# Optimization experiments

Measured on AMD Instinct MI355X. Metric: run time of the kernel, lower is better.

## Reference

```python
import jax, jax.numpy as jnp
import numpy as np

DIM = 768
D_STATE = 64
D_CONV = 4
EXPAND = 2
D_INNER = EXPAND * DIM          # 1536
DT_RANK = (DIM + 15) // 16      # 48
BATCH = 2
SEQ = 1024
EPS = 1e-5


def setup_inputs() -> dict:
    key = jax.random.key(0)
    ks = jax.random.split(key, 10)
    s = 0.02
    x = jax.random.normal(ks[0], (BATCH, SEQ, DIM), dtype=jnp.float32)
    gamma = jnp.ones((DIM,), jnp.float32)
    beta = jnp.zeros((DIM,), jnp.float32)
    W_in = jax.random.normal(ks[1], (2 * D_INNER, DIM), jnp.float32) * s
    conv_w = jax.random.normal(ks[2], (D_INNER, D_CONV), jnp.float32) * s
    conv_b = jnp.zeros((D_INNER,), jnp.float32)
    W_x = jax.random.normal(ks[3], (DT_RANK + 2 * D_STATE, D_INNER), jnp.float32) * s
    W_dt = jax.random.normal(ks[4], (D_INNER, DT_RANK), jnp.float32) * s
    b_dt = jax.random.uniform(ks[5], (D_INNER,), jnp.float32, -4.0, -2.0)  # dt bias ~ log-space init
    # S4D-real init: A_log[d, n] = log(n+1)
    A_log = jnp.log(jnp.broadcast_to(jnp.arange(1, D_STATE + 1, dtype=jnp.float32), (D_INNER, D_STATE)))
    D = jnp.ones((D_INNER,), jnp.float32)
    W_out = jax.random.normal(ks[6], (DIM, D_INNER), jnp.float32) * s
    return {"x": x, "gamma": gamma, "beta": beta, "W_in": W_in,
            "conv_w": conv_w, "conv_b": conv_b, "W_x": W_x,
            "W_dt": W_dt, "b_dt": b_dt, "A_log": A_log, "D": D, "W_out": W_out}


def _silu(v):
    return v * jax.nn.sigmoid(v)


def _mamba_forward(x, gamma, beta, W_in, conv_w, conv_b, W_x, W_dt, b_dt, A_log, D, W_out):
    B, L, _ = x.shape
    # LayerNorm
    mu = jnp.mean(x, axis=-1, keepdims=True)
    var = jnp.mean(jnp.square(x - mu), axis=-1, keepdims=True)
    xn = (x - mu) * jax.lax.rsqrt(var + EPS) * gamma + beta
    # in_proj -> (u, z)
    xz = jnp.einsum('bld,ed->ble', xn, W_in)          # [B, L, 2*D_INNER]
    u, z = jnp.split(xz, 2, axis=-1)                  # each [B, L, D_INNER]
    # depthwise causal conv1d along L
    uc = jnp.transpose(u, (0, 2, 1))                  # [B, C, L]
    uc = jnp.pad(uc, ((0, 0), (0, 0), (D_CONV - 1, 0)))
    kern = conv_w[:, None, :]                         # [C, 1, K]
    uc = jax.lax.conv_general_dilated(
        uc, kern, window_strides=(1,), padding='VALID',
        feature_group_count=D_INNER,
        dimension_numbers=('NCH', 'OIH', 'NCH'))
    uc = uc + conv_b[None, :, None]
    u = _silu(jnp.transpose(uc, (0, 2, 1)))           # [B, L, D_INNER]
    # x_proj -> (dt, Bssm, Cssm)
    x_dbl = jnp.einsum('blc,ec->ble', u, W_x)
    dt = x_dbl[..., :DT_RANK]
    Bssm = x_dbl[..., DT_RANK:DT_RANK + D_STATE]      # [B, L, N]
    Cssm = x_dbl[..., DT_RANK + D_STATE:]             # [B, L, N]
    delta = jax.nn.softplus(jnp.einsum('blr,cr->blc', dt, W_dt) + b_dt)  # [B, L, C]
    A = -jnp.exp(A_log)                               # [C, N]

    # selective scan, time-major
    d_t = jnp.transpose(delta, (1, 0, 2))             # [L, B, C]
    B_t = jnp.transpose(Bssm, (1, 0, 2))              # [L, B, N]
    C_t = jnp.transpose(Cssm, (1, 0, 2))              # [L, B, N]
    u_t = jnp.transpose(u, (1, 0, 2))                 # [L, B, C]

    def step(h, inp):
        d, b, c, uu = inp
        dA = jnp.exp(d[..., None] * A)                # [B, C, N]
        h = dA * h + d[..., None] * b[:, None, :] * uu[..., None]
        y = jnp.sum(h * c[:, None, :], axis=-1) + D * uu
        return h, y

    h0 = jnp.zeros((B, D_INNER, D_STATE), x.dtype)
    _, ys = jax.lax.scan(step, h0, (d_t, B_t, C_t, u_t))
    y = jnp.transpose(ys, (1, 0, 2))                  # [B, L, C]
    y = y * _silu(z)
    return jnp.einsum('blc,dc->bld', y, W_out)


def reference(x, gamma, beta, W_in, conv_w, conv_b, W_x, W_dt, b_dt, A_log, D, W_out):
    return _mamba_forward(x, gamma, beta, W_in, conv_w, conv_b, W_x,
                          W_dt, b_dt, A_log, D, W_out)
```

## Files before the change

kernel.cpp:

```cpp
#include <hip/hip_runtime.h>
#include <math.h>

#define DIMD 768
#define DSTATE 64
#define DINNER 1536
#define DTRANK 48
#define BATCH 2
#define SEQL 1024
#define NTOK (BATCH*SEQL)
#define XDBL_P 192
#define EPSV 1e-5f

typedef __attribute__((ext_vector_type(8))) short bf16x8;
typedef __attribute__((ext_vector_type(4))) float f32x4;

__device__ inline short f2bf(float f) {
  unsigned u = __float_as_uint(f);
  u = u + 0x7FFFu + ((u >> 16) & 1u);
  return (short)(u >> 16);
}

__global__ __launch_bounds__(256) void ln_kernel(const float* __restrict__ x,
                                                 const float* __restrict__ gamma,
                                                 const float* __restrict__ beta,
                                                 short* __restrict__ xnq) {
  int wave = threadIdx.x >> 6;
  int lane = threadIdx.x & 63;
  int row = blockIdx.x * 4 + wave;
  if (row >= NTOK) return;
  const float* xr = x + (size_t)row * DIMD;
  float v[12];
  float s = 0.f, ss = 0.f;
#pragma unroll
  for (int i = 0; i < 12; ++i) {
    v[i] = xr[lane + i*64];
    s += v[i];
    ss += v[i]*v[i];
  }
#pragma unroll
  for (int m = 1; m < 64; m <<= 1) {
    s  += __shfl_xor(s, m);
    ss += __shfl_xor(ss, m);
  }
  float mu   = s * (1.f/DIMD);
  float var  = ss * (1.f/DIMD) - mu*mu;
  float rstd = rsqrtf(var + EPSV);
  short* o = xnq + (size_t)row * DIMD;
#pragma unroll
  for (int i = 0; i < 12; ++i) {
    int j = lane + i*64;
    o[j] = f2bf((v[i] - mu) * rstd * gamma[j] + beta[j]);
  }
}

#define NW_IN  (3072*768)
#define NW_OUT (768*1536)
#define NW_XP  (192*1536)
__global__ __launch_bounds__(256) void cvt_weights_kernel(const float* __restrict__ Win,
                                                          const float* __restrict__ Wout,
                                                          const float* __restrict__ Wx,
                                                          short* __restrict__ qin,
                                                          short* __restrict__ qout,
                                                          short* __restrict__ qx) {
  int idx = blockIdx.x * 256 + threadIdx.x;
  if (idx < NW_IN) { qin[idx] = f2bf(Win[idx]); return; }
  idx -= NW_IN;
  if (idx < NW_OUT) { qout[idx] = f2bf(Wout[idx]); return; }
  idx -= NW_OUT;
  if (idx < NW_XP) {
    int r = idx / 1536;
    qx[idx] = (r < 176) ? f2bf(Wx[idx]) : (short)0;
  }
}

template<int BN>
__global__ __launch_bounds__(256) void gemm_mfma(const short* __restrict__ A,
                                                 const short* __restrict__ B,
                                                 float* __restrict__ C, int ldc,
                                                 int Kfull, int Kchunk, size_t partStride) {
  constexpr int BM = 128, BK = 64;
  constexpr int WN = (BN == 128) ? 2 : 1;
  constexpr int WM = 4 / WN;
  constexpr int MFR = BM / (WM * 16);
  constexpr int NFR = BN / (WN * 16);
  constexpr int BSW = (BN * BK * 2) / 4096;
  __shared__ short As[BM * BK];
  __shared__ short Bs[BN * BK];
  const int tid  = threadIdx.x;
  const int wave = tid >> 6, lane = tid & 63;
  const int m0 = blockIdx.y * BM;
  const int n0 = blockIdx.x * BN;
  const int wm = wave / WN, wn = wave % WN;
  const int kBeg = blockIdx.z * Kchunk;
  const int kEnd = kBeg + Kchunk;
  C += (size_t)blockIdx.z * partStride;

  const short* aSrc = A + (size_t)(m0 + (tid >> 3)) * Kfull + (tid & 7) * 8;
  const short* bSrc = B + (size_t)(n0 + (tid >> 3)) * Kfull + (tid & 7) * 8;

  f32x4 acc[MFR][NFR];
#pragma unroll
  for (int i = 0; i < MFR; ++i)
#pragma unroll
    for (int j = 0; j < NFR; ++j)
      acc[i][j] = (f32x4){0.f, 0.f, 0.f, 0.f};

  for (int k0 = kBeg; k0 < kEnd; k0 += BK) {
#pragma unroll
    for (int s = 0; s < 4; ++s)
      __builtin_amdgcn_global_load_lds(
        (const __attribute__((address_space(1))) void*)(aSrc + (size_t)s*32*Kfull + k0),
        (__attribute__((address_space(3))) void*)((char*)As + s*4096 + wave*1024),
        16, 0, 0);
#pragma unroll
    for (int s = 0; s < BSW; ++s)
      __builtin_amdgcn_global_load_lds(
        (const __attribute__((address_space(1))) void*)(bSrc + (size_t)s*32*Kfull + k0),
        (__attribute__((address_space(3))) void*)((char*)Bs + s*4096 + wave*1024),
        16, 0, 0);
    __syncthreads();

#pragma unroll
    for (int kk = 0; kk < 2; ++kk) {
      bf16x8 af[MFR], bfr[NFR];
#pragma unroll
      for (int i = 0; i < MFR; ++i) {
        int r = wm * (BM / WM) + i * 16 + (lane & 15);
        af[i] = *(const bf16x8*)&As[r * BK + kk * 32 + (lane >> 4) * 8];
      }
#pragma unroll
      for (int j = 0; j < NFR; ++j) {
        int r = wn * (BN / WN) + j * 16 + (lane & 15);
        bfr[j] = *(const bf16x8*)&Bs[r * BK + kk * 32 + (lane >> 4) * 8];
      }
#pragma unroll
      for (int i = 0; i < MFR; ++i)
#pragma unroll
        for (int j = 0; j < NFR; ++j)
          acc[i][j] = __builtin_amdgcn_mfma_f32_16x16x32_bf16(af[i], bfr[j], acc[i][j], 0, 0, 0);
    }
    __syncthreads();
  }

  const int cn = lane & 15, cr4 = (lane >> 4) * 4;
#pragma unroll
  for (int i = 0; i < MFR; ++i)
#pragma unroll
    for (int j = 0; j < NFR; ++j)
#pragma unroll
      for (int r = 0; r < 4; ++r) {
        int m = m0 + wm * (BM / WM) + i * 16 + cr4 + r;
        int n = n0 + wn * (BN / WN) + j * 16 + cn;
        C[(size_t)m * ldc + n] = acc[i][j][r];
      }
}

__global__ __launch_bounds__(256) void reduce4_kernel(const float* __restrict__ p,
                                                      float* __restrict__ outb) {
  const int n4 = NTOK * XDBL_P / 4;
  int i = blockIdx.x * 256 + threadIdx.x;
  if (i >= n4) return;
  const float4* p4 = (const float4*)p;
  float4 a = p4[i];
  float4 b = p4[i + n4];
  float4 c = p4[i + 2*n4];
  float4 d = p4[i + 3*n4];
  float4 r;
  r.x = ((a.x + b.x) + c.x) + d.x;
  r.y = ((a.y + b.y) + c.y) + d.y;
  r.z = ((a.z + b.z) + c.z) + d.z;
  r.w = ((a.w + b.w) + c.w) + d.w;
  ((float4*)outb)[i] = r;
}

template<int ACT>
__global__ __launch_bounds__(256) void gemm_nt(const float* __restrict__ A, int lda,
                                               const float* __restrict__ W, int ldw,
                                               const float* __restrict__ bias,
                                               float* __restrict__ C, int ldc,
                                               int M, int N, int K) {
  __shared__ float Asl[16][68];
  __shared__ float Wsl[16][68];
  int tid = threadIdx.x;
  int m0 = blockIdx.y * 64;
  int n0 = blockIdx.x * 64;
  int lrow = tid >> 2;
  int lq   = tid & 3;
  int tx = tid & 15;
  int ty = tid >> 4;
  float acc[4][4] = {{0.f}};

  for (int k0 = 0; k0 < K; k0 += 16) {
    float4 av = make_float4(0.f,0.f,0.f,0.f);
    int ar = m0 + lrow;
    if (ar < M) av = *(const float4*)(A + (size_t)ar*lda + k0 + lq*4);
    float4 wv = make_float4(0.f,0.f,0.f,0.f);
    int wr = n0 + lrow;
    if (wr < N) wv = *(const float4*)(W + (size_t)wr*ldw + k0 + lq*4);
    __syncthreads();
    Asl[lq*4+0][lrow] = av.x; Asl[lq*4+1][lrow] = av.y;
    Asl[lq*4+2][lrow] = av.z; Asl[lq*4+3][lrow] = av.w;
    Wsl[lq*4+0][lrow] = wv.x; Wsl[lq*4+1][lrow] = wv.y;
    Wsl[lq*4+2][lrow] = wv.z; Wsl[lq*4+3][lrow] = wv.w;
    __syncthreads();
#pragma unroll
    for (int kk = 0; kk < 16; ++kk) {
      float4 a4 = *(const float4*)&Asl[kk][ty*4];
      float4 w4 = *(const float4*)&Wsl[kk][tx*4];
      float a[4] = {a4.x, a4.y, a4.z, a4.w};
      float w[4] = {w4.x, w4.y, w4.z, w4.w};
#pragma unroll
      for (int i = 0; i < 4; ++i)
#pragma unroll
        for (int j = 0; j < 4; ++j)
          acc[i][j] += a[i]*w[j];
    }
  }

#pragma unroll
  for (int i = 0; i < 4; ++i) {
    int m = m0 + ty*4 + i;
    if (m >= M) continue;
    float* crow = C + (size_t)m*ldc;
    float bm = (ACT == 2) ? bias[m] : 0.f;
#pragma unroll
    for (int j = 0; j < 4; ++j) {
      int n = n0 + tx*4 + j;
      if (n >= N) continue;
      float val = acc[i][j];
      if (ACT == 2) {
        val += bm;
        val = (val > 20.f) ? val : log1pf(__expf(val));
      }
      crow[n] = val;
    }
  }
}

__global__ __launch_bounds__(256) void conv_silu_kernel(const float* __restrict__ xz,
                                                        const float* __restrict__ conv_w,
                                                        const float* __restrict__ conv_b,
                                                        float* __restrict__ uT,
                                                        short* __restrict__ ucq) {
  __shared__ float tile[64][65];
  int b  = blockIdx.z;
  int c0 = blockIdx.x * 64;
  int t0 = blockIdx.y * 64;
  int lx = threadIdx.x & 63;
  int ly = threadIdx.x >> 6;
  int c = c0 + lx;
  const int S = 2*DINNER;
  float w0 = conv_w[c*4+0], w1 = conv_w[c*4+1], w2 = conv_w[c*4+2], w3 = conv_w[c*4+3];
  float cb = conv_b[c];
#pragma unroll
  for (int i = 0; i < 16; ++i) {
    int tl = ly*16 + i;
    int t = t0 + tl;
    const float* up = xz + ((size_t)b*SEQL + t) * S + c;
    float acc = cb + up[0]*w3;
    if (t >= 1) acc += up[-1*S]*w2;
    if (t >= 2) acc += up[-2*S]*w1;
    if (t >= 3) acc += up[-3*S]*w0;
    float sig = 1.f / (1.f + __expf(-acc));
    float v = acc * sig;
    ucq[((size_t)b*SEQL + t)*DINNER + c] = f2bf(v);
    tile[lx][tl] = v;
  }
  __syncthreads();
#pragma unroll
  for (int i = 0; i < 16; ++i) {
    int cl = ly*16 + i;
    uT[((size_t)(c0 + cl))*NTOK + (size_t)b*SEQL + t0 + lx] = tile[cl][lx];
  }
}

__device__ inline float readlane_f(float v, int l) {
  return __int_as_float(__builtin_amdgcn_readlane(__float_as_int(v), l));
}

__global__ __launch_bounds__(256) void scan_kernel(const float* __restrict__ dT,
                                                   const float* __restrict__ x_dbl,
                                                   const float* __restrict__ uT,
                                                   const float* __restrict__ A_log,
                                                   const float* __restrict__ Dp,
                                                   float* __restrict__ yT) {
  __shared__ float red_all[4][32*66 + 32];
  int tid  = threadIdx.x;
  int wave = tid >> 6;
  int lane = tid & 63;
  float* red = red_all[wave];
  int ch = blockIdx.x * 4 + wave;
  int b = ch / DINNER;
  int c = ch % DINNER;
  float Ac = -__expf(A_log[(size_t)c*64 + lane]);
  float Dc = Dp[c];
  float h = 0.f;
  const float* dp = dT + (size_t)c * NTOK + (size_t)b * SEQL;
  const float* up = uT + (size_t)c * NTOK + (size_t)b * SEQL;
  float* yrow = yT + ((size_t)b*DINNER + c) * SEQL;
  const float* xB = x_dbl + ((size_t)b * SEQL) * XDBL_P + DTRANK + lane;

  float d_v = dp[lane];
  float u_v = up[lane];

  const int r = lane & 31, hs = lane >> 5;
  const int NBLK = SEQL/64;
  for (int tb = 0; tb < NBLK; ++tb) {
    int t0 = tb*64;
    float d_nxt = 0.f, u_nxt = 0.f;
    if (tb + 1 < NBLK) {
      d_nxt = dp[t0 + 64 + lane];
      u_nxt = up[t0 + 64 + lane];
    }
    float du_v = d_v * u_v;

#pragma unroll
    for (int half = 0; half < 2; ++half) {
      const float* xh = xB + (size_t)(t0 + half*32) * XDBL_P;
#pragma unroll
      for (int k = 0; k < 32; ++k) {
        int i = half*32 + k;
        float Bv = xh[(size_t)k * XDBL_P];
        float Cv = xh[(size_t)k * XDBL_P + DSTATE];
        float sd  = readlane_f(d_v,  i);
        float sdu = readlane_f(du_v, i);
        float dA = __expf(sd * Ac);
        h = fmaf(dA, h, sdu * Bv);
        red[k*66 + lane] = h * Cv;
      }
      {
        const float2* rp2 = (const float2*)&red[r*66 + hs*32];
        float2 a0 = rp2[0], a1 = rp2[1];
#pragma unroll
        for (int jj = 1; jj < 8; ++jj) {
          float2 v0 = rp2[2*jj], v1 = rp2[2*jj + 1];
          a0.x += v0.x; a0.y += v0.y;
          a1.x += v1.x; a1.y += v1.y;
        }
        float y = (a0.x + a0.y) + (a1.x + a1.y);
        y += __shfl_xor(y, 32);
        float ut = __shfl(u_v, half*32 + r);
        y = fmaf(Dc, ut, y);
        if (lane < 32) yrow[t0 + half*32 + lane] = y;
      }
    }
    __syncthreads();
    d_v = d_nxt;
    u_v = u_nxt;
  }
}

__global__ __launch_bounds__(256) void ymul_kernel(const float* __restrict__ yT,
                                                   const float* __restrict__ xz,
                                                   short* __restrict__ g) {
  __shared__ float tile[64][65];
  int b  = blockIdx.z;
  int c0 = blockIdx.x * 64;
  int t0 = blockIdx.y * 64;
  int lx = threadIdx.x & 63;
  int ly = threadIdx.x >> 6;
  const float* src = yT + ((size_t)b*DINNER + c0) * SEQL + t0;
#pragma unroll
  for (int i = 0; i < 16; ++i) {
    int c = ly*16 + i;
    tile[c][lx] = src[(size_t)c*SEQL + lx];
  }
  __syncthreads();
  const int S = 2*DINNER;
#pragma unroll
  for (int i = 0; i < 16; ++i) {
    int t = ly*16 + i;
    float z = xz[((size_t)b*SEQL + t0 + t)*S + DINNER + c0 + lx];
    float zs = z / (1.f + __expf(-z));
    g[((size_t)b*SEQL + t0 + t)*DINNER + c0 + lx] = f2bf(tile[lx][t] * zs);
  }
}

extern "C" void kernel_launch(void* const* d_in, const int* in_sizes, int n_in,
                              void* d_out, int out_size, void* d_ws, size_t ws_size,
                              hipStream_t stream) {
  const float* x      = (const float*)d_in[0];
  const float* gamma  = (const float*)d_in[1];
  const float* beta   = (const float*)d_in[2];
  const float* W_in   = (const float*)d_in[3];
  const float* conv_w = (const float*)d_in[4];
  const float* conv_b = (const float*)d_in[5];
  const float* W_x    = (const float*)d_in[6];
  const float* W_dt   = (const float*)d_in[7];
  const float* b_dt   = (const float*)d_in[8];
  const float* A_log  = (const float*)d_in[9];
  const float* Dvec   = (const float*)d_in[10];
  const float* W_out  = (const float*)d_in[11];
  float* out = (float*)d_out;

  float* ws = (float*)d_ws;
  float* xz    = ws;
  float* uT    = xz    + (size_t)NTOK*3072;
  float* xdbl  = uT    + (size_t)NTOK*1536;
  float* dltT  = xdbl  + (size_t)NTOK*XDBL_P;
  float* yT    = dltT  + (size_t)NTOK*1536;
  float* xpart = yT    + (size_t)NTOK*1536;
  short* xnq   = (short*)(xpart + (size_t)4*NTOK*XDBL_P);
  short* ucq   = xnq  + (size_t)NTOK*768;
  short* gq    = ucq  + (size_t)NTOK*1536;
  short* qin   = gq   + (size_t)NTOK*1536;
  short* qx    = qin  + (size_t)NW_IN;
  short* qout  = qx   + (size_t)NW_XP;

  cvt_weights_kernel<<<(NW_IN+NW_OUT+NW_XP+255)/256, 256, 0, stream>>>(W_in, W_out, W_x, qin, qout, qx);
  ln_kernel<<<NTOK/4, 256, 0, stream>>>(x, gamma, beta, xnq);
  gemm_mfma<64><<<dim3(3072/64, NTOK/128), 256, 0, stream>>>(xnq, qin, xz, 3072, DIMD, DIMD, 0);
  conv_silu_kernel<<<dim3(DINNER/64, SEQL/64, BATCH), 256, 0, stream>>>(xz, conv_w, conv_b, uT, ucq);
  gemm_mfma<64><<<dim3(XDBL_P/64, NTOK/128, 4), 256, 0, stream>>>(ucq, qx, xpart, XDBL_P,
                                                                  DINNER, DINNER/4,
                                                                  (size_t)NTOK*XDBL_P);
  reduce4_kernel<<<(NTOK*XDBL_P/4 + 255)/256, 256, 0, stream>>>(xpart, xdbl);
  gemm_nt<2><<<dim3(NTOK/64, DINNER/64), 256, 0, stream>>>(W_dt, DTRANK, xdbl, XDBL_P, b_dt,
                                                           dltT, NTOK, DINNER, NTOK, DTRANK);
  scan_kernel<<<BATCH*DINNER/4, 256, 0, stream>>>(dltT, xdbl, uT, A_log, Dvec, yT);
  ymul_kernel<<<dim3(DINNER/64, SEQL/64, BATCH), 256, 0, stream>>>(yT, xz, gq);
  gemm_mfma<64><<<dim3(DIMD/64, NTOK/128), 256, 0, stream>>>(gq, qout, out, DIMD, DINNER, DINNER, 0);
}
```

Measured before the change: 196.5 us.

## Interleave B/C projection rows, slide conv window, use exp2 in scan

Permutes the x_proj weight rows so the B and C outputs come out interleaved per state index, which lets the scan fetch both with one float2 load instead of two scalar loads. The scan also folds log2(e) into A so it can call the hardware exp2 directly. The depthwise conv keeps a sliding window of the previous three inputs in registers, so each timestep does one global load instead of four. The layout change ties the weight conversion to the scan's indexing, so any other consumer of the B/C columns must match the new order.

```diff
diff --git a/kernel.cpp b/kernel.cpp
--- a/kernel.cpp
+++ b/kernel.cpp
@@ -68,8 +68,14 @@
   if (idx < NW_OUT) { qout[idx] = f2bf(Wout[idx]); return; }
   idx -= NW_OUT;
   if (idx < NW_XP) {
-    int r = idx / 1536;
-    qx[idx] = (r < 176) ? f2bf(Wx[idx]) : (short)0;
+    int r = idx / 1536, col = idx % 1536;
+    int srcr;
+    if (r < 48) srcr = r;
+    else if (r < 176) {
+      int n = r - 48;
+      srcr = (n & 1) ? 112 + (n >> 1) : 48 + (n >> 1);
+    } else srcr = -1;
+    qx[idx] = (srcr >= 0) ? f2bf(Wx[(size_t)srcr * 1536 + col]) : (short)0;
   }
 }
 
@@ -252,19 +258,20 @@
   const int S = 2*DINNER;
   float w0 = conv_w[c*4+0], w1 = conv_w[c*4+1], w2 = conv_w[c*4+2], w3 = conv_w[c*4+3];
   float cb = conv_b[c];
+  int ts = t0 + ly*16;
+  const float* col = xz + ((size_t)b*SEQL + ts) * S + c;
+  float x3 = (ts >= 3) ? col[-3*S] : 0.f;
+  float x2 = (ts >= 2) ? col[-2*S] : 0.f;
+  float x1 = (ts >= 1) ? col[-1*S] : 0.f;
 #pragma unroll
   for (int i = 0; i < 16; ++i) {
-    int tl = ly*16 + i;
-    int t = t0 + tl;
-    const float* up = xz + ((size_t)b*SEQL + t) * S + c;
-    float acc = cb + up[0]*w3;
-    if (t >= 1) acc += up[-1*S]*w2;
-    if (t >= 2) acc += up[-2*S]*w1;
-    if (t >= 3) acc += up[-3*S]*w0;
+    float x0 = col[(size_t)i*S];
+    float acc = cb + x3*w0 + x2*w1 + x1*w2 + x0*w3;
     float sig = 1.f / (1.f + __expf(-acc));
     float v = acc * sig;
-    ucq[((size_t)b*SEQL + t)*DINNER + c] = f2bf(v);
-    tile[lx][tl] = v;
+    ucq[((size_t)b*SEQL + ts + i)*DINNER + c] = f2bf(v);
+    tile[lx][ly*16 + i] = v;
+    x3 = x2; x2 = x1; x1 = x0;
   }
   __syncthreads();
 #pragma unroll
@@ -292,13 +299,13 @@
   int ch = blockIdx.x * 4 + wave;
   int b = ch / DINNER;
   int c = ch % DINNER;
-  float Ac = -__expf(A_log[(size_t)c*64 + lane]);
+  float Ac2 = -__expf(A_log[(size_t)c*64 + lane]) * 1.44269504f;
   float Dc = Dp[c];
   float h = 0.f;
   const float* dp = dT + (size_t)c * NTOK + (size_t)b * SEQL;
   const float* up = uT + (size_t)c * NTOK + (size_t)b * SEQL;
   float* yrow = yT + ((size_t)b*DINNER + c) * SEQL;
-  const float* xB = x_dbl + ((size_t)b * SEQL) * XDBL_P + DTRANK + lane;
+  const float* xBC = x_dbl + ((size_t)b * SEQL) * XDBL_P + DTRANK + 2*lane;
 
   float d_v = dp[lane];
   float u_v = up[lane];
@@ -316,17 +323,16 @@
 
 #pragma unroll
     for (int half = 0; half < 2; ++half) {
-      const float* xh = xB + (size_t)(t0 + half*32) * XDBL_P;
+      const float* xh = xBC + (size_t)(t0 + half*32) * XDBL_P;
 #pragma unroll
       for (int k = 0; k < 32; ++k) {
         int i = half*32 + k;
-        float Bv = xh[(size_t)k * XDBL_P];
-        float Cv = xh[(size_t)k * XDBL_P + DSTATE];
+        float2 BC = *(const float2*)&xh[(size_t)k * XDBL_P];
         float sd  = readlane_f(d_v,  i);
         float sdu = readlane_f(du_v, i);
-        float dA = __expf(sd * Ac);
-        h = fmaf(dA, h, sdu * Bv);
-        red[k*66 + lane] = h * Cv;
+        float dA = __builtin_amdgcn_exp2f(sd * Ac2);
+        h = fmaf(dA, h, sdu * BC.x);
+        red[k*66 + lane] = h * BC.y;
       }
       {
         const float2* rp2 = (const float2*)&red[r*66 + hs*32];
```

Result: slower. 207.5 us (+5.6%).
